# Kernel optimization log

Measured on AMD Instinct MI355X. Metric: run time of the kernel, lower is better.

Reference implementation:

```python
import jax, jax.numpy as jnp
import numpy as np

B, S, D = 4, 2048, 1024
H = 16
DH = D // H          # 64
DFF = 4096
EPS = 1e-5


def _layer_norm(x, gamma, beta):
    mu = jnp.mean(x, axis=-1, keepdims=True)
    var = jnp.mean(jnp.square(x - mu), axis=-1, keepdims=True)
    return (x - mu) * jax.lax.rsqrt(var + EPS) * gamma + beta


def setup_inputs() -> dict:
    key = jax.random.key(0)
    ks = jax.random.split(key, 8)
    s_in = 1.0 / np.sqrt(D)
    s_ff = 1.0 / np.sqrt(DFF)
    return {
        "x": jax.random.normal(ks[0], (B, S, D), dtype=jnp.float32),
        # per-head qkv weights stacked: [H, D, 3*DH] (nn.Linear, bias=False)
        "Wqkv": jax.random.normal(ks[1], (H, D, 3 * DH), dtype=jnp.float32) * s_in,
        "Wproj": jax.random.normal(ks[2], (D, D), dtype=jnp.float32) * s_in,
        "bproj": jnp.zeros((D,), dtype=jnp.float32),
        "ln1_g": jnp.ones((D,), dtype=jnp.float32),
        "ln1_b": jnp.zeros((D,), dtype=jnp.float32),
        "ln2_g": jnp.ones((D,), dtype=jnp.float32),
        "ln2_b": jnp.zeros((D,), dtype=jnp.float32),
        "W1": jax.random.normal(ks[3], (D, DFF), dtype=jnp.float32) * s_in,
        "b1": jnp.zeros((DFF,), dtype=jnp.float32),
        "W2": jax.random.normal(ks[4], (DFF, D), dtype=jnp.float32) * s_ff,
        "b2": jnp.zeros((D,), dtype=jnp.float32),
    }


def reference(x, Wqkv, Wproj, bproj, ln1_g, ln1_b, ln2_g, ln2_b, W1, b1, W2, b2):
    # fused multi-head QKV projection: [B,S,D] x [H,D,3*DH] -> [B,H,S,3*DH]
    qkv = jnp.einsum('bsd,hde->bhse', x, Wqkv)
    q, k, v = jnp.split(qkv, 3, axis=-1)          # each [B,H,S,DH]
    scale = 1.0 / jnp.sqrt(jnp.asarray(DH, dtype=x.dtype))
    scores = jnp.einsum('bhsd,bhtd->bhst', q, k) * scale   # [B,H,S,S]
    causal = jnp.tril(jnp.ones((S, S), dtype=bool))
    scores = jnp.where(causal, scores, jnp.finfo(x.dtype).min)
    attn = jax.nn.softmax(scores, axis=-1)
    heads = jnp.einsum('bhst,bhtd->bhsd', attn, v)          # [B,H,S,DH]
    att_out = heads.transpose(0, 2, 1, 3).reshape(B, S, D)  # concat heads
    att_out = att_out @ Wproj + bproj
    out = _layer_norm(x + att_out, ln1_g, ln1_b)            # dropout = identity (eval)
    mlp_out = (jax.nn.gelu(out @ W1 + b1, approximate=False)) @ W2 + b2
    out = _layer_norm(out + mlp_out, ln2_g, ln2_b)
    return out
```

## Files before the change

kernel.cpp:

```cpp
#include <hip/hip_runtime.h>
#include <math.h>

#define BB 4
#define SS 2048
#define DD 1024
#define HH 16
#define DHH 64
#define DFF 4096
static constexpr float LN_EPS = 1e-5f;

typedef __bf16 bf16x8 __attribute__((ext_vector_type(8)));
typedef float f32x4 __attribute__((ext_vector_type(4)));
typedef unsigned short u16x8 __attribute__((ext_vector_type(8)));

__device__ __forceinline__ unsigned short f2bf(float f) {
    return __builtin_bit_cast(unsigned short, (__bf16)f);
}

__device__ __forceinline__ float fexp2(float x) {
    return __builtin_amdgcn_exp2f(x);
}

__device__ __forceinline__ void gl_lds16(const unsigned short* g,
                                         unsigned short* l) {
    __builtin_amdgcn_global_load_lds(
        (const __attribute__((address_space(1))) unsigned int*)g,
        (__attribute__((address_space(3))) unsigned int*)l, 16, 0, 0);
}

#define GBAR()                               \
    do {                                     \
        asm volatile("" ::: "memory");       \
        __builtin_amdgcn_s_barrier();        \
        asm volatile("" ::: "memory");       \
    } while (0)
#define VMCNT(n) asm volatile("s_waitcnt vmcnt(" #n ")" ::: "memory")

__global__ __launch_bounds__(256) void transpose_bf16_kernel(
    const float* __restrict__ in, unsigned short* __restrict__ outT,
    int R, int C) {
    __shared__ float t[64][65];
    const int r0 = blockIdx.y * 64, c0 = blockIdx.x * 64;
    const int cl = threadIdx.x & 63, rl = threadIdx.x >> 6;
#pragma unroll
    for (int rr = 0; rr < 16; ++rr)
        t[rl + rr * 4][cl] = in[(size_t)(r0 + rl + rr * 4) * C + c0 + cl];
    __syncthreads();
#pragma unroll
    for (int rr = 0; rr < 16; ++rr)
        outT[(size_t)(c0 + rl + rr * 4) * R + r0 + cl] = f2bf(t[cl][rl + rr * 4]);
}

__global__ __launch_bounds__(256) void repack_wqkv_bf16_kernel(
    const float* __restrict__ Wqkv, unsigned short* __restrict__ Wq2T) {
    __shared__ float t[64][65];
    const int h = blockIdx.z;
    const int d0 = blockIdx.y * 64, e0 = blockIdx.x * 64;
    const int cl = threadIdx.x & 63, rl = threadIdx.x >> 6;
#pragma unroll
    for (int rr = 0; rr < 16; ++rr)
        t[rl + rr * 4][cl] =
            Wqkv[((size_t)h * DD + d0 + rl + rr * 4) * 192 + e0 + cl];
    __syncthreads();
#pragma unroll
    for (int rr = 0; rr < 16; ++rr)
        Wq2T[((size_t)h * 192 + e0 + rl + rr * 4) * DD + d0 + cl] =
            f2bf(t[cl][rl + rr * 4]);
}

__global__ __launch_bounds__(256) void f2bf_kernel(
    const float* __restrict__ in, unsigned short* __restrict__ out, int n) {
    int i = blockIdx.x * 256 + threadIdx.x;
    if (i < n) out[i] = f2bf(in[i]);
}

template <int RS>
__device__ __forceinline__ void stage_half(const unsigned short* __restrict__ G,
                                           int ldK, int growbase, int kbase,
                                           unsigned short* lbase, int tid) {
#pragma unroll
    for (int s = 0; s < 2; ++s) {
        const int c16 = s * 512 + tid;
        const int r = c16 >> 3, c = c16 & 7;
        const int grow =
            growbase + ((r >> RS) << (RS + 1)) + (r & ((1 << RS) - 1));
        const int gcol = kbase + ((c ^ (r & 7)) << 3);
        gl_lds16(&G[(size_t)grow * ldK + gcol], &lbase[c16 << 3]);
    }
}

__device__ __forceinline__ void stage_64(const unsigned short* __restrict__ G,
                                         int ldK, int growbase, int kbase,
                                         unsigned short* lbase, int tid) {
    const int r = tid >> 3, c = tid & 7;
    const int grow = growbase + ((r >> 5) << 6) + (r & 31);
    const int gcol = kbase + ((c ^ (r & 7)) << 3);
    gl_lds16(&G[(size_t)grow * ldK + gcol], &lbase[tid << 3]);
}

__device__ __forceinline__ void stage_kv(const unsigned short* __restrict__ src,
                                         size_t rstride, unsigned short* dst,
                                         int tid) {
#pragma unroll
    for (int s = 0; s < 2; ++s) {
        const int c16 = s * 256 + tid;
        const int r = c16 >> 3, c = c16 & 7;
        gl_lds16(&src[(size_t)r * rstride + ((c ^ (r & 7)) << 3)],
                 &dst[c16 << 3]);
    }
}

__device__ __forceinline__ void read_afrag(const unsigned short* s, int base,
                                           int wm, int l15, int g,
                                           bf16x8 af[4][2]) {
#pragma unroll
    for (int ii = 0; ii < 4; ++ii) {
        const int lr = wm * 64 + ii * 16 + l15;
#pragma unroll
        for (int ks = 0; ks < 2; ++ks) {
            const int p = ((ks << 2) + g) ^ (lr & 7);
            af[ii][ks] = __builtin_bit_cast(
                bf16x8, *(const u16x8*)&s[base + lr * 64 + p * 8]);
        }
    }
}

__device__ __forceinline__ void read_bfrag(const unsigned short* s, int base,
                                           int wn, int l15, int g,
                                           bf16x8 bf2[2][2]) {
#pragma unroll
    for (int jj = 0; jj < 2; ++jj) {
        const int lr = wn * 32 + jj * 16 + l15;
#pragma unroll
        for (int ks = 0; ks < 2; ++ks) {
            const int p = ((ks << 2) + g) ^ (lr & 7);
            bf2[jj][ks] = __builtin_bit_cast(
                bf16x8, *(const u16x8*)&s[base + lr * 64 + p * 8]);
        }
    }
}

template <int MH, int NH>
__device__ __forceinline__ void mfma_quad(f32x4 acc[8][4],
                                          const bf16x8 af[4][2],
                                          const bf16x8 bf2[2][2]) {
    __builtin_amdgcn_s_setprio(1);
#pragma unroll
    for (int ks = 0; ks < 2; ++ks)
#pragma unroll
        for (int ii = 0; ii < 4; ++ii)
#pragma unroll
            for (int jj = 0; jj < 2; ++jj)
                acc[MH * 4 + ii][NH * 2 + jj] =
                    __builtin_amdgcn_mfma_f32_16x16x32_bf16(
                        af[ii][ks], bf2[jj][ks],
                        acc[MH * 4 + ii][NH * 2 + jj], 0, 0, 0);
    __builtin_amdgcn_s_setprio(0);
}

template <int MODE>
__global__ __launch_bounds__(512) void mfma_gemm256_kernel(
    const unsigned short* __restrict__ A, const unsigned short* __restrict__ BT,
    float* __restrict__ Cf, unsigned short* __restrict__ Cb,
    const float* __restrict__ bias, const float* __restrict__ resid,
    int M, int N, int K) {
    __shared__ __align__(16) unsigned short smem[65536];
    const int tid = threadIdx.x;
    const int lane = tid & 63, wave = tid >> 6;
    const int wm = wave >> 2, wn = wave & 3;
    const int l15 = lane & 15, g = lane >> 4;

    const int gx = gridDim.x, nwg = gx * gridDim.y;
    const int lid = blockIdx.y * gx + blockIdx.x;
    const int swz = ((nwg & 7) == 0) ? ((lid & 7) * (nwg >> 3) + (lid >> 3))
                                     : lid;
    const int row0 = (swz / gx) * 256;
    const int col0 = (swz % gx) * 256;

    const int kt = K >> 6;

    f32x4 acc[8][4] = {};

    stage_half<6>(A, K, row0, 0, smem + 0, tid);
    stage_half<6>(A, K, row0 + 64, 0, smem + 8192, tid);
    stage_half<5>(BT, K, col0, 0, smem + 32768, tid);
    stage_half<5>(BT, K, col0 + 32, 0, smem + 40960, tid);
    VMCNT(4);
    stage_half<6>(A, K, row0, 64, smem + 16384, tid);
    stage_half<6>(A, K, row0 + 64, 64, smem + 24576, tid);
    stage_half<5>(BT, K, col0, 64, smem + 49152, tid);
    VMCNT(6);
    GBAR();

    bf16x8 af[4][2], bf0[2][2], bf1[2][2];
    for (int it = 0; it < (kt >> 1); ++it) {
        const int t1k = (2 * it + 1) << 6;
        int t2 = 2 * it + 2; if (t2 > kt - 1) t2 = kt - 1;
        int t3 = 2 * it + 3; if (t3 > kt - 1) t3 = kt - 1;
        const int t2k = t2 << 6, t3k = t3 << 6;

        read_afrag(smem, 0, wm, l15, g, af);
        read_bfrag(smem, 32768, wn, l15, g, bf0);
        stage_half<5>(BT, K, col0 + 32, t1k, smem + 57344, tid);
        GBAR();
        mfma_quad<0, 0>(acc, af, bf0);
        GBAR();

        read_bfrag(smem, 40960, wn, l15, g, bf1);
        stage_half<6>(A, K, row0, t2k, smem + 0, tid);
        GBAR();
        mfma_quad<0, 1>(acc, af, bf1);
        GBAR();

        read_afrag(smem, 8192, wm, l15, g, af);
        stage_half<5>(BT, K, col0, t2k, smem + 32768, tid);
        GBAR();
        mfma_quad<1, 1>(acc, af, bf1);
        GBAR();

        stage_half<6>(A, K, row0 + 64, t2k, smem + 8192, tid);
        GBAR();
        mfma_quad<1, 0>(acc, af, bf0);
        VMCNT(6);
        GBAR();

        read_afrag(smem, 16384, wm, l15, g, af);
        read_bfrag(smem, 49152, wn, l15, g, bf0);
        stage_half<5>(BT, K, col0 + 32, t2k, smem + 40960, tid);
        GBAR();
        mfma_quad<0, 0>(acc, af, bf0);
        GBAR();

        read_bfrag(smem, 57344, wn, l15, g, bf1);
        stage_half<6>(A, K, row0, t3k, smem + 16384, tid);
        GBAR();
        mfma_quad<0, 1>(acc, af, bf1);
        GBAR();

        read_afrag(smem, 24576, wm, l15, g, af);
        stage_half<5>(BT, K, col0, t3k, smem + 49152, tid);
        GBAR();
        mfma_quad<1, 1>(acc, af, bf1);
        GBAR();

        stage_half<6>(A, K, row0 + 64, t3k, smem + 24576, tid);
        GBAR();
        mfma_quad<1, 0>(acc, af, bf0);
        VMCNT(6);
        GBAR();
    }
    VMCNT(0);
    GBAR();

    if (MODE == 2) {
        constexpr int SLAB = 264;
#pragma unroll
        for (int i2 = 0; i2 < 8; ++i2) {
            __syncthreads();
#pragma unroll
            for (int j2 = 0; j2 < 4; ++j2) {
                const int col = wn * 64 + j2 * 16 + l15;
                const float bv = bias[col0 + col];
#pragma unroll
                for (int r = 0; r < 4; ++r) {
                    float v = acc[i2][j2][r] + bv;
                    float t = fexp2(v * (2.30211849f + 0.10294198f * v * v));
                    float gel = v * t * __builtin_amdgcn_rcpf(t + 1.f);
                    smem[(wm * 16 + g * 4 + r) * SLAB + col] = f2bf(gel);
                }
            }
            __syncthreads();
            const int sr = tid >> 4;
            const int cc = (tid & 15) * 16;
            const int grow = row0 + ((sr >> 4) << 7) + i2 * 16 + (sr & 15);
            *(u16x8*)&Cb[(size_t)grow * N + col0 + cc] =
                *(const u16x8*)&smem[sr * SLAB + cc];
            *(u16x8*)&Cb[(size_t)grow * N + col0 + cc + 8] =
                *(const u16x8*)&smem[sr * SLAB + cc + 8];
        }
        return;
    }

#pragma unroll
    for (int i2 = 0; i2 < 8; ++i2) {
#pragma unroll
        for (int j2 = 0; j2 < 4; ++j2) {
            const int col = col0 + wn * 64 + j2 * 16 + l15;
            const int rowb = row0 + wm * 128 + i2 * 16 + g * 4;
            const float bv = bias[col];
#pragma unroll
            for (int r = 0; r < 4; ++r) {
                const int row = rowb + r;
                float v = acc[i2][j2][r] + bv + resid[(size_t)row * N + col];
                Cf[(size_t)row * N + col] = v;
            }
        }
    }
}

__device__ __forceinline__ void read_af128(const unsigned short* s, int base,
                                           int wm, int l15, int g,
                                           bf16x8 af[2][2]) {
#pragma unroll
    for (int ii = 0; ii < 2; ++ii) {
        const int lr = wm * 32 + ii * 16 + l15;
#pragma unroll
        for (int ks = 0; ks < 2; ++ks) {
            const int p = ((ks << 2) + g) ^ (lr & 7);
            af[ii][ks] = __builtin_bit_cast(
                bf16x8, *(const u16x8*)&s[base + lr * 64 + p * 8]);
        }
    }
}

__device__ __forceinline__ void read_bf128(const unsigned short* s, int base,
                                           int wn, int l15, int g,
                                           bf16x8 bf2[2][2]) {
#pragma unroll
    for (int jj = 0; jj < 2; ++jj) {
        const int lr = wn * 32 + jj * 16 + l15;
#pragma unroll
        for (int ks = 0; ks < 2; ++ks) {
            const int p = ((ks << 2) + g) ^ (lr & 7);
            bf2[jj][ks] = __builtin_bit_cast(
                bf16x8, *(const u16x8*)&s[base + lr * 64 + p * 8]);
        }
    }
}

template <int MH, int NH>
__device__ __forceinline__ void mfma_quad128(f32x4 acc[4][4],
                                             const bf16x8 af[2][2],
                                             const bf16x8 bf2[2][2]) {
    __builtin_amdgcn_s_setprio(1);
#pragma unroll
    for (int ks = 0; ks < 2; ++ks)
#pragma unroll
        for (int ii = 0; ii < 2; ++ii)
#pragma unroll
            for (int jj = 0; jj < 2; ++jj)
                acc[MH * 2 + ii][NH * 2 + jj] =
                    __builtin_amdgcn_mfma_f32_16x16x32_bf16(
                        af[ii][ks], bf2[jj][ks],
                        acc[MH * 2 + ii][NH * 2 + jj], 0, 0, 0);
    __builtin_amdgcn_s_setprio(0);
}

template <int MODE>
__global__ __launch_bounds__(512) void gemm_n128_kernel(
    const unsigned short* __restrict__ A, const unsigned short* __restrict__ BT,
    float* __restrict__ Cf, const float* __restrict__ bias,
    const float* __restrict__ resid, unsigned short* __restrict__ Qb,
    unsigned short* __restrict__ Kb, unsigned short* __restrict__ VTb,
    int M, int N, int K) {
    __shared__ __align__(16) unsigned short smem[49152];
    const int tid = threadIdx.x;
    const int lane = tid & 63, wave = tid >> 6;
    const int wm = wave >> 1, wn = wave & 1;
    const int l15 = lane & 15, g = lane >> 4;

    const int gx = gridDim.x, nwg = gx * gridDim.y;
    const int lid = blockIdx.y * gx + blockIdx.x;
    const int swz = ((nwg & 7) == 0) ? ((lid & 7) * (nwg >> 3) + (lid >> 3))
                                     : lid;
    const int row0 = (swz / gx) * 256;
    const int col0 = (swz % gx) * 128;

    const int kt = K >> 6;

    f32x4 acc[4][4] = {};

    stage_half<5>(A, K, row0, 0, smem + 0, tid);
    stage_half<5>(A, K, row0 + 32, 0, smem + 8192, tid);
    stage_64(BT, K, col0, 0, smem + 32768, tid);
    stage_64(BT, K, col0 + 32, 0, smem + 36864, tid);
    VMCNT(4);
    stage_half<5>(A, K, row0, 64, smem + 16384, tid);
    stage_half<5>(A, K, row0 + 32, 64, smem + 24576, tid);
    stage_64(BT, K, col0, 64, smem + 40960, tid);
    VMCNT(5);
    GBAR();

    bf16x8 af[2][2], bf0[2][2], bf1[2][2];
    for (int it = 0; it < (kt >> 1); ++it) {
        const int t1k = (2 * it + 1) << 6;
        int t2 = 2 * it + 2; if (t2 > kt - 1) t2 = kt - 1;
        int t3 = 2 * it + 3; if (t3 > kt - 1) t3 = kt - 1;
        const int t2k = t2 << 6, t3k = t3 << 6;

        read_af128(smem, 0, wm, l15, g, af);
        read_bf128(smem, 32768, wn, l15, g, bf0);
        stage_64(BT, K, col0 + 32, t1k, smem + 45056, tid);
        GBAR();
        mfma_quad128<0, 0>(acc, af, bf0);
        GBAR();

        read_bf128(smem, 36864, wn, l15, g, bf1);
        stage_half<5>(A, K, row0, t2k, smem + 0, tid);
        GBAR();
        mfma_quad128<0, 1>(acc, af, bf1);
        GBAR();

        read_af128(smem, 8192, wm, l15, g, af);
        stage_64(BT, K, col0, t2k, smem + 32768, tid);
        GBAR();
        mfma_quad128<1, 1>(acc, af, bf1);
        GBAR();

        stage_half<5>(A, K, row0 + 32, t2k, smem + 8192, tid);
        GBAR();
        mfma_quad128<1, 0>(acc, af, bf0);
        VMCNT(5);
        GBAR();

        read_af128(smem, 16384, wm, l15, g, af);
        read_bf128(smem, 40960, wn, l15, g, bf0);
        stage_64(BT, K, col0 + 32, t2k, smem + 36864, tid);
        GBAR();
        mfma_quad128<0, 0>(acc, af, bf0);
        GBAR();

        read_bf128(smem, 45056, wn, l15, g, bf1);
        stage_half<5>(A, K, row0, t3k, smem + 16384, tid);
        GBAR();
        mfma_quad128<0, 1>(acc, af, bf1);
        GBAR();

        read_af128(smem, 24576, wm, l15, g, af);
        stage_64(BT, K, col0, t3k, smem + 40960, tid);
        GBAR();
        mfma_quad128<1, 1>(acc, af, bf1);
        GBAR();

        stage_half<5>(A, K, row0 + 32, t3k, smem + 24576, tid);
        GBAR();
        mfma_quad128<1, 0>(acc, af, bf0);
        VMCNT(5);
        GBAR();
    }
    VMCNT(0);
    GBAR();

#pragma unroll
    for (int i2 = 0; i2 < 4; ++i2) {
#pragma unroll
        for (int j2 = 0; j2 < 4; ++j2) {
            const int col = col0 + wn * 64 + j2 * 16 + l15;
            const int rowb = row0 + wm * 64 + i2 * 16 + g * 4;
            if (MODE == 4) {
                const int h = col / 192, e = col % 192;
                const int bb = rowb >> 11, s = rowb & 2047;
                if (e < 64) {
                    unsigned short* q =
                        Qb + (((size_t)bb * HH + h) * SS + s) * 64 + e;
#pragma unroll
                    for (int r = 0; r < 4; ++r)
                        q[r * 64] = f2bf(acc[i2][j2][r] * 0.18033688f);
                } else if (e < 128) {
                    unsigned short* kp =
                        Kb + (((size_t)bb * HH + h) * SS + s) * 64 + (e - 64);
#pragma unroll
                    for (int r = 0; r < 4; ++r)
                        kp[r * 64] = f2bf(acc[i2][j2][r]);
                } else {
                    ushort4 pk;
                    pk.x = f2bf(acc[i2][j2][0]);
                    pk.y = f2bf(acc[i2][j2][1]);
                    pk.z = f2bf(acc[i2][j2][2]);
                    pk.w = f2bf(acc[i2][j2][3]);
                    *(ushort4*)(VTb + (((size_t)bb * HH + h) * 64 + (e - 128)) *
                                          SS + s) = pk;
                }
            } else {
                const float bv = bias[col];
#pragma unroll
                for (int r = 0; r < 4; ++r) {
                    const int row = rowb + r;
                    float v = acc[i2][j2][r] + bv + resid[(size_t)row * N + col];
                    Cf[(size_t)row * N + col] = v;
                }
            }
        }
    }
}

__global__ __launch_bounds__(256) void fattn_kernel(
    const unsigned short* __restrict__ Qb, const unsigned short* __restrict__ Kb,
    const unsigned short* __restrict__ VTb, unsigned short* __restrict__ att) {
    constexpr int PSTR = 68;
    __shared__ __align__(16) unsigned short Pls[128 * PSTR];
    __shared__ __align__(16) unsigned short Kls[2][64 * 64];
    __shared__ __align__(16) unsigned short VTls[2][64 * 64];

    const int bh = blockIdx.x;
    const int q0 = blockIdx.y * 128;
    const int tid = threadIdx.x;
    const int lane = tid & 63;
    const int wave = tid >> 6;
    const int l15 = lane & 15;
    const int g = lane >> 4;
    const int b = bh >> 4, h = bh & 15;

    const unsigned short* Qh = Qb + (size_t)bh * SS * 64;
    const unsigned short* Kh = Kb + (size_t)bh * SS * 64;
    const unsigned short* Vh = VTb + (size_t)bh * 64 * SS;

    {
        const int row = tid >> 1, c0 = (tid & 1) * 32;
        const unsigned short* src = Qh + (size_t)(q0 + row) * 64 + c0;
        unsigned short* dst = &Pls[row * PSTR + c0];
#pragma unroll
        for (int c = 0; c < 32; c += 8)
            *(u16x8*)(dst + c) = *(const u16x8*)(src + c);
    }
    bf16x8 qf[2][2];
#pragma unroll
    for (int i = 0; i < 2; ++i)
#pragma unroll
        for (int ks = 0; ks < 2; ++ks)
            qf[i][ks] = __builtin_bit_cast(
                bf16x8, *(const u16x8*)&Pls[(wave * 32 + i * 16 + l15) * PSTR +
                                            ks * 32 + g * 8]);

    f32x4 oacc[4][2] = {};
    float mst[2], lst[2];
#pragma unroll
    for (int i = 0; i < 2; ++i) { mst[i] = -1e30f; lst[i] = 0.f; }

    const int qlim = q0 + wave * 32 + 31;
    const int qrow = wave * 32 + l15;
    const int nt = (q0 >> 6) + 2;
    const int xh = l15 & 7;

    stage_kv(Kh, 64, &Kls[0][0], tid);
    stage_kv(Vh, SS, &VTls[0][0], tid);

    for (int t = 0; t < nt; ++t) {
        const int t0 = t << 6;
        const int tn = (t + 1 < nt) ? t + 1 : nt - 1;
        stage_kv(Kh + (size_t)(tn << 6) * 64, 64, &Kls[(t + 1) & 1][0], tid);
        stage_kv(Vh + (tn << 6), SS, &VTls[(t + 1) & 1][0], tid);
        VMCNT(4);
        GBAR();

        if (t0 <= qlim) {
            const unsigned short* Kt = &Kls[t & 1][0];
            const unsigned short* Vt = &VTls[t & 1][0];

            f32x4 sacc[4][2] = {};
#pragma unroll
            for (int ks = 0; ks < 2; ++ks) {
                const int ko = ((((ks << 2) + g) ^ xh) << 3);
                bf16x8 kb[4];
#pragma unroll
                for (int j = 0; j < 4; ++j)
                    kb[j] = __builtin_bit_cast(
                        bf16x8, *(const u16x8*)&Kt[(j * 16 + l15) * 64 + ko]);
#pragma unroll
                for (int j = 0; j < 4; ++j)
#pragma unroll
                    for (int i = 0; i < 2; ++i)
                        sacc[j][i] = __builtin_amdgcn_mfma_f32_16x16x32_bf16(
                            kb[j], qf[i][ks], sacc[j][i], 0, 0, 0);
            }

            if (t0 >= q0) {
#pragma unroll
                for (int j = 0; j < 4; ++j)
#pragma unroll
                    for (int i = 0; i < 2; ++i)
#pragma unroll
                        for (int r = 0; r < 4; ++r) {
                            const int kg = t0 + j * 16 + g * 4 + r;
                            const int qg = q0 + qrow + i * 16;
                            if (kg > qg) sacc[j][i][r] = -1e30f;
                        }
            }

#pragma unroll
            for (int i = 0; i < 2; ++i) {
                float mx = -1e30f;
#pragma unroll
                for (int j = 0; j < 4; ++j)
                    mx = fmaxf(mx,
                               fmaxf(fmaxf(sacc[j][i][0], sacc[j][i][1]),
                                     fmaxf(sacc[j][i][2], sacc[j][i][3])));
                mx = fmaxf(mx, __shfl_xor(mx, 16));
                mx = fmaxf(mx, __shfl_xor(mx, 32));
                const bool grow = !__all(mx <= mst[i]);
                float al = 1.f;
                if (grow) {
                    const float mn = fmaxf(mst[i], mx);
                    al = fexp2(mst[i] - mn);
                    mst[i] = mn;
                }
                const float mm = mst[i];
                float rsum = 0.f;
                const int pbase = (qrow + i * 16) * PSTR + g * 4;
#pragma unroll
                for (int j = 0; j < 4; ++j) {
                    float p0 = fexp2(sacc[j][i][0] - mm);
                    float p1 = fexp2(sacc[j][i][1] - mm);
                    float p2 = fexp2(sacc[j][i][2] - mm);
                    float p3 = fexp2(sacc[j][i][3] - mm);
                    rsum += (p0 + p1) + (p2 + p3);
                    ushort4 pk;
                    pk.x = f2bf(p0); pk.y = f2bf(p1);
                    pk.z = f2bf(p2); pk.w = f2bf(p3);
                    *(ushort4*)&Pls[pbase + j * 16] = pk;
                }
                rsum += __shfl_xor(rsum, 16);
                rsum += __shfl_xor(rsum, 32);
                if (grow) {
                    lst[i] = lst[i] * al + rsum;
#pragma unroll
                    for (int jo = 0; jo < 4; ++jo)
#pragma unroll
                        for (int r = 0; r < 4; ++r) oacc[jo][i][r] *= al;
                } else {
                    lst[i] += rsum;
                }
            }

#pragma unroll
            for (int ks = 0; ks < 2; ++ks) {
                const int ko = ((((ks << 2) + g) ^ xh) << 3);
                bf16x8 vb[4], pf[2];
#pragma unroll
                for (int jo = 0; jo < 4; ++jo)
                    vb[jo] = __builtin_bit_cast(
                        bf16x8, *(const u16x8*)&Vt[(jo * 16 + l15) * 64 + ko]);
#pragma unroll
                for (int i = 0; i < 2; ++i)
                    pf[i] = __builtin_bit_cast(
                        bf16x8, *(const u16x8*)&Pls[(qrow + i * 16) * PSTR +
                                                    ks * 32 + g * 8]);
#pragma unroll
                for (int jo = 0; jo < 4; ++jo)
#pragma unroll
                    for (int i = 0; i < 2; ++i)
                        oacc[jo][i] = __builtin_amdgcn_mfma_f32_16x16x32_bf16(
                            vb[jo], pf[i], oacc[jo][i], 0, 0, 0);
            }
        }
        GBAR();
    }
    VMCNT(0);

#pragma unroll
    for (int i = 0; i < 2; ++i) {
        const float inv = 1.f / lst[i];
        const int qg = q0 + qrow + i * 16;
        unsigned short* dst = att + ((size_t)b * SS + qg) * DD + h * 64 + g * 4;
#pragma unroll
        for (int jo = 0; jo < 4; ++jo) {
            ushort4 pk;
            pk.x = f2bf(oacc[jo][i][0] * inv);
            pk.y = f2bf(oacc[jo][i][1] * inv);
            pk.z = f2bf(oacc[jo][i][2] * inv);
            pk.w = f2bf(oacc[jo][i][3] * inv);
            *(ushort4*)(dst + jo * 16) = pk;
        }
    }
}

__global__ __launch_bounds__(256) void ln_kernel(
    const float* __restrict__ X, const float* __restrict__ g,
    const float* __restrict__ bta, float* __restrict__ Y,
    unsigned short* __restrict__ Yb) {
    const int row = blockIdx.x;
    const float4 xv = ((const float4*)(X + (size_t)row * DD))[threadIdx.x];

    __shared__ float red1[4], red2[4];
    float s = xv.x + xv.y + xv.z + xv.w;
#pragma unroll
    for (int off = 32; off > 0; off >>= 1) s += __shfl_down(s, off);
    const int wave = threadIdx.x >> 6;
    if ((threadIdx.x & 63) == 0) red1[wave] = s;
    __syncthreads();
    const float mu = (red1[0] + red1[1] + red1[2] + red1[3]) * (1.f / DD);

    float dx = xv.x - mu, dy = xv.y - mu, dz = xv.z - mu, dw = xv.w - mu;
    float s2 = dx * dx + dy * dy + dz * dz + dw * dw;
#pragma unroll
    for (int off = 32; off > 0; off >>= 1) s2 += __shfl_down(s2, off);
    if ((threadIdx.x & 63) == 0) red2[wave] = s2;
    __syncthreads();
    const float var = (red2[0] + red2[1] + red2[2] + red2[3]) * (1.f / DD);
    const float rstd = rsqrtf(var + LN_EPS);

    const float4 gv = ((const float4*)g)[threadIdx.x];
    const float4 bv = ((const float4*)bta)[threadIdx.x];
    float4 yv;
    yv.x = dx * rstd * gv.x + bv.x;
    yv.y = dy * rstd * gv.y + bv.y;
    yv.z = dz * rstd * gv.z + bv.z;
    yv.w = dw * rstd * gv.w + bv.w;
    ((float4*)(Y + (size_t)row * DD))[threadIdx.x] = yv;
    if (Yb) {
        ushort4 q;
        q.x = f2bf(yv.x); q.y = f2bf(yv.y);
        q.z = f2bf(yv.z); q.w = f2bf(yv.w);
        ((ushort4*)(Yb + (size_t)row * DD))[threadIdx.x] = q;
    }
}

extern "C" void kernel_launch(void* const* d_in, const int* in_sizes, int n_in,
                              void* d_out, int out_size, void* d_ws,
                              size_t ws_size, hipStream_t stream) {
    const float* x     = (const float*)d_in[0];
    const float* Wqkv  = (const float*)d_in[1];
    const float* Wproj = (const float*)d_in[2];
    const float* bproj = (const float*)d_in[3];
    const float* ln1_g = (const float*)d_in[4];
    const float* ln1_b = (const float*)d_in[5];
    const float* ln2_g = (const float*)d_in[6];
    const float* ln2_b = (const float*)d_in[7];
    const float* W1    = (const float*)d_in[8];
    const float* b1    = (const float*)d_in[9];
    const float* W2    = (const float*)d_in[10];
    const float* b2    = (const float*)d_in[11];
    float* out = (float*)d_out;

    const size_t M = (size_t)BB * SS;
    const size_t MB = 1024 * 1024;
    char* w = (char*)d_ws;
    unsigned short* Qb     = (unsigned short*)(w + 0);
    unsigned short* out1b  = (unsigned short*)(w + 0);
    unsigned short* Kb     = (unsigned short*)(w + 16 * MB);
    unsigned short* VTb    = (unsigned short*)(w + 32 * MB);
    unsigned short* hbuf   = (unsigned short*)(w + 16 * MB);
    unsigned short* Wq2T   = (unsigned short*)(w + 96 * MB);
    unsigned short* xb     = (unsigned short*)(w + 102 * MB);
    unsigned short* att    = (unsigned short*)(w + 96 * MB);
    float*          out1   = (float*)(w + 96 * MB);
    unsigned short* WprojT = (unsigned short*)(w + 118 * MB);
    unsigned short* W1T    = (unsigned short*)(w + 128 * MB);
    unsigned short* W2T    = (unsigned short*)(w + 136 * MB);

    repack_wqkv_bf16_kernel<<<dim3(3, 16, 16), 256, 0, stream>>>(Wqkv, Wq2T);
    transpose_bf16_kernel<<<dim3(16, 16), 256, 0, stream>>>(Wproj, WprojT, 1024, 1024);
    transpose_bf16_kernel<<<dim3(64, 16), 256, 0, stream>>>(W1, W1T, 1024, 4096);
    transpose_bf16_kernel<<<dim3(16, 64), 256, 0, stream>>>(W2, W2T, 4096, 1024);
    f2bf_kernel<<<(int)((M * DD + 255) / 256), 256, 0, stream>>>(x, xb, (int)(M * DD));

    gemm_n128_kernel<4><<<dim3(3072 / 128, M / 256), 512, 0, stream>>>(
        xb, Wq2T, nullptr, nullptr, nullptr, Qb, Kb, VTb, (int)M, 3072, 1024);

    fattn_kernel<<<dim3(BB * HH, SS / 128), 256, 0, stream>>>(Qb, Kb, VTb, att);

    gemm_n128_kernel<3><<<dim3(1024 / 128, M / 256), 512, 0, stream>>>(
        att, WprojT, out, bproj, x, nullptr, nullptr, nullptr,
        (int)M, 1024, 1024);

    ln_kernel<<<(int)M, 256, 0, stream>>>(out, ln1_g, ln1_b, out1, out1b);

    mfma_gemm256_kernel<2><<<dim3(4096 / 256, M / 256), 512, 0, stream>>>(
        out1b, W1T, nullptr, hbuf, b1, nullptr, (int)M, 4096, 1024);

    gemm_n128_kernel<3><<<dim3(1024 / 128, M / 256), 512, 0, stream>>>(
        hbuf, W2T, out, b2, out1, nullptr, nullptr, nullptr,
        (int)M, 1024, 4096);

    ln_kernel<<<(int)M, 256, 0, stream>>>(out, ln2_g, ln2_b, out, nullptr);
}
```

Before: 505.3 us.

## Pair causal attention query chunks per block and keep P in registers

Each attention block now processes two query chunks (p and 15-p) so that causal work is balanced across the halved grid. K rows are staged with a permuted order so the S-accumulator layout matches the B-operand layout of the PV MFMA, which lets P be packed into registers instead of going through an LDS round-trip. It also drops the Q staging buffer, adds s_setprio around the MFMA blocks and sets launch_bounds occupancy to 2. The risks are fewer blocks in flight, the serialized pair of chunks per block, and added register pressure.

```diff
diff --git a/kernel.cpp b/kernel.cpp
--- a/kernel.cpp
+++ b/kernel.cpp
@@ -12,6 +12,7 @@
 typedef __bf16 bf16x8 __attribute__((ext_vector_type(8)));
 typedef float f32x4 __attribute__((ext_vector_type(4)));
 typedef unsigned short u16x8 __attribute__((ext_vector_type(8)));
+typedef unsigned int u32x4 __attribute__((ext_vector_type(4)));
 
 __device__ __forceinline__ unsigned short f2bf(float f) {
     return __builtin_bit_cast(unsigned short, (__bf16)f);
@@ -106,6 +107,19 @@
         const int c16 = s * 256 + tid;
         const int r = c16 >> 3, c = c16 & 7;
         gl_lds16(&src[(size_t)r * rstride + ((c ^ (r & 7)) << 3)],
+                 &dst[c16 << 3]);
+    }
+}
+
+__device__ __forceinline__ void stage_k_pi(const unsigned short* __restrict__ src,
+                                           unsigned short* dst, int tid) {
+#pragma unroll
+    for (int s = 0; s < 2; ++s) {
+        const int c16 = s * 256 + tid;
+        const int r = c16 >> 3, c = c16 & 7;
+        const int gr = ((r >> 4) & 1) * 32 + (((r >> 2) & 3) << 3) +
+                       ((r >> 5) & 1) * 4 + (r & 3);
+        gl_lds16(&src[(size_t)gr * 64 + ((c ^ (r & 7)) << 3)],
                  &dst[c16 << 3]);
     }
 }
@@ -484,183 +498,195 @@
     }
 }
 
-__global__ __launch_bounds__(256) void fattn_kernel(
+__global__ __launch_bounds__(256, 2) void fattn_kernel(
     const unsigned short* __restrict__ Qb, const unsigned short* __restrict__ Kb,
     const unsigned short* __restrict__ VTb, unsigned short* __restrict__ att) {
-    constexpr int PSTR = 68;
-    __shared__ __align__(16) unsigned short Pls[128 * PSTR];
     __shared__ __align__(16) unsigned short Kls[2][64 * 64];
     __shared__ __align__(16) unsigned short VTls[2][64 * 64];
 
     const int bh = blockIdx.x;
-    const int q0 = blockIdx.y * 128;
+    const int p = blockIdx.y;
     const int tid = threadIdx.x;
     const int lane = tid & 63;
     const int wave = tid >> 6;
     const int l15 = lane & 15;
     const int g = lane >> 4;
     const int b = bh >> 4, h = bh & 15;
+    const int xh = l15 & 7;
 
     const unsigned short* Qh = Qb + (size_t)bh * SS * 64;
     const unsigned short* Kh = Kb + (size_t)bh * SS * 64;
     const unsigned short* Vh = VTb + (size_t)bh * 64 * SS;
 
-    {
-        const int row = tid >> 1, c0 = (tid & 1) * 32;
-        const unsigned short* src = Qh + (size_t)(q0 + row) * 64 + c0;
-        unsigned short* dst = &Pls[row * PSTR + c0];
-#pragma unroll
-        for (int c = 0; c < 32; c += 8)
-            *(u16x8*)(dst + c) = *(const u16x8*)(src + c);
-    }
-    bf16x8 qf[2][2];
-#pragma unroll
-    for (int i = 0; i < 2; ++i)
-#pragma unroll
-        for (int ks = 0; ks < 2; ++ks)
-            qf[i][ks] = __builtin_bit_cast(
-                bf16x8, *(const u16x8*)&Pls[(wave * 32 + i * 16 + l15) * PSTR +
-                                            ks * 32 + g * 8]);
-
-    f32x4 oacc[4][2] = {};
-    float mst[2], lst[2];
-#pragma unroll
-    for (int i = 0; i < 2; ++i) { mst[i] = -1e30f; lst[i] = 0.f; }
-
-    const int qlim = q0 + wave * 32 + 31;
-    const int qrow = wave * 32 + l15;
-    const int nt = (q0 >> 6) + 2;
-    const int xh = l15 & 7;
-
-    stage_kv(Kh, 64, &Kls[0][0], tid);
-    stage_kv(Vh, SS, &VTls[0][0], tid);
-
-    for (int t = 0; t < nt; ++t) {
-        const int t0 = t << 6;
-        const int tn = (t + 1 < nt) ? t + 1 : nt - 1;
-        stage_kv(Kh + (size_t)(tn << 6) * 64, 64, &Kls[(t + 1) & 1][0], tid);
-        stage_kv(Vh + (tn << 6), SS, &VTls[(t + 1) & 1][0], tid);
-        VMCNT(4);
-        GBAR();
-
-        if (t0 <= qlim) {
-            const unsigned short* Kt = &Kls[t & 1][0];
-            const unsigned short* Vt = &VTls[t & 1][0];
-
-            f32x4 sacc[4][2] = {};
-#pragma unroll
-            for (int ks = 0; ks < 2; ++ks) {
-                const int ko = ((((ks << 2) + g) ^ xh) << 3);
-                bf16x8 kb[4];
-#pragma unroll
-                for (int j = 0; j < 4; ++j)
-                    kb[j] = __builtin_bit_cast(
-                        bf16x8, *(const u16x8*)&Kt[(j * 16 + l15) * 64 + ko]);
-#pragma unroll
-                for (int j = 0; j < 4; ++j)
-#pragma unroll
-                    for (int i = 0; i < 2; ++i)
-                        sacc[j][i] = __builtin_amdgcn_mfma_f32_16x16x32_bf16(
-                            kb[j], qf[i][ks], sacc[j][i], 0, 0, 0);
+#pragma unroll 1
+    for (int half = 0; half < 2; ++half) {
+        const int cidx = half ? (15 - p) : p;
+        const int q0c = cidx << 7;
+        const int qw = q0c + wave * 32;
+        const int qlim = qw + 31;
+        const int nt = (cidx << 1) + 2;
+
+        bf16x8 qf[2][2];
+#pragma unroll
+        for (int i = 0; i < 2; ++i)
+#pragma unroll
+            for (int ks = 0; ks < 2; ++ks)
+                qf[i][ks] = __builtin_bit_cast(
+                    bf16x8, *(const u16x8*)&Qh[(size_t)(qw + i * 16 + l15) * 64 +
+                                               ks * 32 + g * 8]);
+
+        f32x4 oacc[4][2] = {};
+        float mst[2], lst[2];
+#pragma unroll
+        for (int i = 0; i < 2; ++i) { mst[i] = -1e30f; lst[i] = 0.f; }
+
+        stage_k_pi(Kh, &Kls[0][0], tid);
+        stage_kv(Vh, SS, &VTls[0][0], tid);
+
+        for (int t = 0; t < nt; ++t) {
+            const int t0 = t << 6;
+            if (t + 1 < nt) {
+                stage_k_pi(Kh + ((size_t)(t + 1) << 6) * 64,
+                           &Kls[(t + 1) & 1][0], tid);
+                stage_kv(Vh + ((t + 1) << 6), SS, &VTls[(t + 1) & 1][0], tid);
+                VMCNT(4);
+            } else {
+                VMCNT(0);
             }
-
-            if (t0 >= q0) {
-#pragma unroll
-                for (int j = 0; j < 4; ++j)
-#pragma unroll
-                    for (int i = 0; i < 2; ++i)
-#pragma unroll
-                        for (int r = 0; r < 4; ++r) {
-                            const int kg = t0 + j * 16 + g * 4 + r;
-                            const int qg = q0 + qrow + i * 16;
-                            if (kg > qg) sacc[j][i][r] = -1e30f;
+            GBAR();
+
+            if (t0 <= qlim) {
+                const unsigned short* Kt = &Kls[t & 1][0];
+                const unsigned short* Vt = &VTls[t & 1][0];
+
+                f32x4 sacc[4][2] = {};
+                __builtin_amdgcn_s_setprio(1);
+#pragma unroll
+                for (int ks = 0; ks < 2; ++ks) {
+                    const int ko = ((((ks << 2) + g) ^ xh) << 3);
+                    bf16x8 kb[4];
+#pragma unroll
+                    for (int j = 0; j < 4; ++j)
+                        kb[j] = __builtin_bit_cast(
+                            bf16x8,
+                            *(const u16x8*)&Kt[(j * 16 + l15) * 64 + ko]);
+#pragma unroll
+                    for (int j = 0; j < 4; ++j)
+#pragma unroll
+                        for (int i = 0; i < 2; ++i)
+                            sacc[j][i] =
+                                __builtin_amdgcn_mfma_f32_16x16x32_bf16(
+                                    kb[j], qf[i][ks], sacc[j][i], 0, 0, 0);
+                }
+                __builtin_amdgcn_s_setprio(0);
+
+                if (t0 + 63 > qw) {
+#pragma unroll
+                    for (int j = 0; j < 4; ++j) {
+                        const int kgb = t0 + ((j & 1) << 5) + (g << 3) +
+                                        ((j >> 1) << 2);
+#pragma unroll
+                        for (int i = 0; i < 2; ++i) {
+                            const int qgi = qw + i * 16 + l15;
+#pragma unroll
+                            for (int r = 0; r < 4; ++r)
+                                if (kgb + r > qgi) sacc[j][i][r] = -1e30f;
                         }
-            }
-
-#pragma unroll
-            for (int i = 0; i < 2; ++i) {
-                float mx = -1e30f;
-#pragma unroll
-                for (int j = 0; j < 4; ++j)
-                    mx = fmaxf(mx,
-                               fmaxf(fmaxf(sacc[j][i][0], sacc[j][i][1]),
-                                     fmaxf(sacc[j][i][2], sacc[j][i][3])));
-                mx = fmaxf(mx, __shfl_xor(mx, 16));
-                mx = fmaxf(mx, __shfl_xor(mx, 32));
-                const bool grow = !__all(mx <= mst[i]);
-                float al = 1.f;
-                if (grow) {
-                    const float mn = fmaxf(mst[i], mx);
-                    al = fexp2(mst[i] - mn);
-                    mst[i] = mn;
+                    }
                 }
-                const float mm = mst[i];
-                float rsum = 0.f;
-                const int pbase = (qrow + i * 16) * PSTR + g * 4;
-#pragma unroll
-                for (int j = 0; j < 4; ++j) {
-                    float p0 = fexp2(sacc[j][i][0] - mm);
-                    float p1 = fexp2(sacc[j][i][1] - mm);
-                    float p2 = fexp2(sacc[j][i][2] - mm);
-                    float p3 = fexp2(sacc[j][i][3] - mm);
-                    rsum += (p0 + p1) + (p2 + p3);
-                    ushort4 pk;
-                    pk.x = f2bf(p0); pk.y = f2bf(p1);
-                    pk.z = f2bf(p2); pk.w = f2bf(p3);
-                    *(ushort4*)&Pls[pbase + j * 16] = pk;
+
+                unsigned int Aw[2][4], Bw[2][4];
+#pragma unroll
+                for (int i = 0; i < 2; ++i) {
+                    float mx = -1e30f;
+#pragma unroll
+                    for (int j = 0; j < 4; ++j)
+                        mx = fmaxf(mx,
+                                   fmaxf(fmaxf(sacc[j][i][0], sacc[j][i][1]),
+                                         fmaxf(sacc[j][i][2], sacc[j][i][3])));
+                    mx = fmaxf(mx, __shfl_xor(mx, 16));
+                    mx = fmaxf(mx, __shfl_xor(mx, 32));
+                    const bool grow = !__all(mx <= mst[i]);
+                    float al = 1.f;
+                    if (grow) {
+                        const float mn = fmaxf(mst[i], mx);
+                        al = fexp2(mst[i] - mn);
+                        mst[i] = mn;
+                    }
+                    const float mm = mst[i];
+                    float rsum = 0.f;
+#pragma unroll
+                    for (int j = 0; j < 4; ++j) {
+                        float p0 = fexp2(sacc[j][i][0] - mm);
+                        float p1 = fexp2(sacc[j][i][1] - mm);
+                        float p2 = fexp2(sacc[j][i][2] - mm);
+                        float p3 = fexp2(sacc[j][i][3] - mm);
+                        rsum += (p0 + p1) + (p2 + p3);
+                        Aw[i][j] = (unsigned int)f2bf(p0) |
+                                   ((unsigned int)f2bf(p1) << 16);
+                        Bw[i][j] = (unsigned int)f2bf(p2) |
+                                   ((unsigned int)f2bf(p3) << 16);
+                    }
+                    rsum += __shfl_xor(rsum, 16);
+                    rsum += __shfl_xor(rsum, 32);
+                    if (grow) {
+                        lst[i] = lst[i] * al + rsum;
+#pragma unroll
+                        for (int jo = 0; jo < 4; ++jo)
+#pragma unroll
+                            for (int r = 0; r < 4; ++r) oacc[jo][i][r] *= al;
+                    } else {
+                        lst[i] += rsum;
+                    }
                 }
-                rsum += __shfl_xor(rsum, 16);
-                rsum += __shfl_xor(rsum, 32);
-                if (grow) {
-                    lst[i] = lst[i] * al + rsum;
+
+#pragma unroll
+                for (int ks = 0; ks < 2; ++ks) {
+                    const int ko = ((((ks << 2) + g) ^ xh) << 3);
+                    bf16x8 vb[4];
 #pragma unroll
                     for (int jo = 0; jo < 4; ++jo)
-#pragma unroll
-                        for (int r = 0; r < 4; ++r) oacc[jo][i][r] *= al;
-                } else {
-                    lst[i] += rsum;
+                        vb[jo] = __builtin_bit_cast(
+                            bf16x8,
+                            *(const u16x8*)&Vt[(jo * 16 + l15) * 64 + ko]);
+                    __builtin_amdgcn_s_setprio(1);
+#pragma unroll
+                    for (int i = 0; i < 2; ++i) {
+                        u32x4 pw;
+                        pw[0] = Aw[i][ks];
+                        pw[1] = Bw[i][ks];
+                        pw[2] = Aw[i][2 + ks];
+                        pw[3] = Bw[i][2 + ks];
+                        const bf16x8 pf = __builtin_bit_cast(bf16x8, pw);
+#pragma unroll
+                        for (int jo = 0; jo < 4; ++jo)
+                            oacc[jo][i] =
+                                __builtin_amdgcn_mfma_f32_16x16x32_bf16(
+                                    vb[jo], pf, oacc[jo][i], 0, 0, 0);
+                    }
+                    __builtin_amdgcn_s_setprio(0);
                 }
             }
-
-#pragma unroll
-            for (int ks = 0; ks < 2; ++ks) {
-                const int ko = ((((ks << 2) + g) ^ xh) << 3);
-                bf16x8 vb[4], pf[2];
-#pragma unroll
-                for (int jo = 0; jo < 4; ++jo)
-                    vb[jo] = __builtin_bit_cast(
-                        bf16x8, *(const u16x8*)&Vt[(jo * 16 + l15) * 64 + ko]);
-#pragma unroll
-                for (int i = 0; i < 2; ++i)
-                    pf[i] = __builtin_bit_cast(
-                        bf16x8, *(const u16x8*)&Pls[(qrow + i * 16) * PSTR +
-                                                    ks * 32 + g * 8]);
-#pragma unroll
-                for (int jo = 0; jo < 4; ++jo)
-#pragma unroll
-                    for (int i = 0; i < 2; ++i)
-                        oacc[jo][i] = __builtin_amdgcn_mfma_f32_16x16x32_bf16(
-                            vb[jo], pf[i], oacc[jo][i], 0, 0, 0);
+            GBAR();
+        }
+
+#pragma unroll
+        for (int i = 0; i < 2; ++i) {
+            const float inv = 1.f / lst[i];
+            const int qg = qw + i * 16 + l15;
+            unsigned short* dst =
+                att + ((size_t)b * SS + qg) * DD + h * 64 + g * 4;
+#pragma unroll
+            for (int jo = 0; jo < 4; ++jo) {
+                ushort4 pk;
+                pk.x = f2bf(oacc[jo][i][0] * inv);
+                pk.y = f2bf(oacc[jo][i][1] * inv);
+                pk.z = f2bf(oacc[jo][i][2] * inv);
+                pk.w = f2bf(oacc[jo][i][3] * inv);
+                *(ushort4*)(dst + jo * 16) = pk;
             }
         }
         GBAR();
-    }
-    VMCNT(0);
-
-#pragma unroll
-    for (int i = 0; i < 2; ++i) {
-        const float inv = 1.f / lst[i];
-        const int qg = q0 + qrow + i * 16;
-        unsigned short* dst = att + ((size_t)b * SS + qg) * DD + h * 64 + g * 4;
-#pragma unroll
-        for (int jo = 0; jo < 4; ++jo) {
-            ushort4 pk;
-            pk.x = f2bf(oacc[jo][i][0] * inv);
-            pk.y = f2bf(oacc[jo][i][1] * inv);
-            pk.z = f2bf(oacc[jo][i][2] * inv);
-            pk.w = f2bf(oacc[jo][i][3] * inv);
-            *(ushort4*)(dst + jo * 16) = pk;
-        }
     }
 }
 
@@ -747,7 +773,7 @@
     gemm_n128_kernel<4><<<dim3(3072 / 128, M / 256), 512, 0, stream>>>(
         xb, Wq2T, nullptr, nullptr, nullptr, Qb, Kb, VTb, (int)M, 3072, 1024);
 
-    fattn_kernel<<<dim3(BB * HH, SS / 128), 256, 0, stream>>>(Qb, Kb, VTb, att);
+    fattn_kernel<<<dim3(BB * HH, 8), 256, 0, stream>>>(Qb, Kb, VTb, att);
 
     gemm_n128_kernel<3><<<dim3(1024 / 128, M / 256), 512, 0, stream>>>(
         att, WprojT, out, bproj, x, nullptr, nullptr, nullptr,
```

Result: faster. 477.5 us (-5.5%).
